# Kernel optimization log

Measured on AMD Instinct MI355X. Metric: run time of the kernel, lower is better.

## Reference

```python
import jax, jax.numpy as jnp
import numpy as np
from jax import lax

# pywt db4 filters. REC_LO is pywt's rec_lo; the others follow pywt's QMF relations:
# rec_hi[k] = (-1)**k * rec_lo[F-1-k]; dec_lo = rec_lo[::-1]; dec_hi = rec_hi[::-1].
REC_LO = np.array([0.23037781330885523, 0.7148465705525415, 0.6308807679295904,
                   -0.027983769416983849, -0.18703481171888114, 0.030841381835986965,
                   0.032883011666982945, -0.010597401784997278], dtype=np.float32)
F = 8
REC_HI = np.array([(-1.0) ** k * REC_LO[F - 1 - k] for k in range(F)], dtype=np.float32)
DEC_LO = REC_LO[::-1].copy()
DEC_HI = REC_HI[::-1].copy()
LEVELS = 3


def _conv(x, kern, stride=1, lhs_dilation=1, padding=((0, 0),)):
    # x: (N, 1, L) ; 1-D correlation (jax conv does NOT flip the kernel)
    k = jnp.asarray(kern, x.dtype).reshape(1, 1, -1)
    return lax.conv_general_dilated(x, k, window_strides=(stride,), padding=padding,
                                    lhs_dilation=(lhs_dilation,),
                                    dimension_numbers=('NCH', 'OIH', 'NCH'))


def dwt(x):
    # pywt single-level dwt, mode='symmetric': extend by F-1 each side, then
    # decimated convolution with dec filters. Equivalent to: drop first extended
    # sample and stride-2 correlate with reversed dec filter (= rec filter).
    xe = jnp.pad(x, ((0, 0), (0, 0), (F - 1, F - 1)), mode='symmetric')[..., 1:]
    cA = _conv(xe, REC_LO, stride=2)   # rev(DEC_LO) == REC_LO
    cD = _conv(xe, REC_HI, stride=2)   # rev(DEC_HI) == REC_HI
    return cA, cD


def idwt(a, d):
    # pywt idwt: upsample by 2 (zeros between samples, len 2L-1), full-convolve
    # with rec filters, trim F-2 from each side -> len 2L - F + 2.
    # Via dilated conv: lhs_dilation=2, pad 1 each side, correlate with rev(rec)=dec.
    ra = _conv(a, DEC_LO, lhs_dilation=2, padding=((1, 1),))
    rd = _conv(d, DEC_HI, lhs_dilation=2, padding=((1, 1),))
    return ra + rd


def waverec(coeffs):
    a = coeffs[0]
    for d in coeffs[1:]:
        if a.shape[-1] == d.shape[-1] + 1:
            a = a[..., :-1]
        a = idwt(a, d)
    return a


def setup_inputs() -> dict:
    key = jax.random.key(0)
    x = jax.random.normal(key, (32, 64, 8192), dtype=jnp.float32)
    return {"x": x}


def reference(x):
    B, C, n = x.shape
    a = x.reshape(B * C, 1, n)
    details = []
    for _ in range(LEVELS):
        a, d = dwt(a)
        details.append(d)
    coeffs = [a] + details[::-1]  # [cA_L, cD_L, ..., cD_1] as in pywt.wavedec
    bands = []
    for i in range(LEVELS + 1):
        kept = [c if j == i else jnp.zeros_like(c) for j, c in enumerate(coeffs)]
        rec = waverec(kept)[..., :n]
        bands.append(rec.reshape(B, C, n))
    return tuple(bands)
```

## Files before the change

### kernel.cpp

```cpp
#include <hip/hip_runtime.h>


#define T     256
#define N0    8192
#define L1    4099
#define L2    2053
#define L3    1030
#define NROWS 2048

#define RL0 0.23037781330885523f
#define RL1 0.7148465705525415f
#define RL2 0.6308807679295904f
#define RL3 (-0.02798376941698385f)
#define RL4 (-0.18703481171888114f)
#define RL5 0.030841381835986965f
#define RL6 0.032883011666982945f
#define RL7 (-0.010597401784997278f)

__device__ __forceinline__ void fwd_level(const float* __restrict__ src, int n, int Lout,
                                          float* __restrict__ dstA, float* __restrict__ dstD,
                                          int tid)
{
    const float lo[8] = {RL0, RL1, RL2, RL3, RL4, RL5, RL6, RL7};
    const float hi[8] = {RL7, -RL6, RL5, -RL4, RL3, -RL2, RL1, -RL0};
    for (int i = tid; i < Lout; i += T) {
        int j0 = 2 * i - 6;
        float sa = 0.f, sd = 0.f;
#pragma unroll
        for (int t = 0; t < 8; ++t) {
            int m = j0 + t;
            m = (m < 0) ? (-1 - m) : m;
            m = (m >= n) ? (2 * n - 1 - m) : m;
            float v = src[m];
            sa = fmaf(v, lo[t], sa);
            sd = fmaf(v, hi[t], sd);
        }
        dstA[i] = sa;
        dstD[i] = sd;
    }
}

__device__ __forceinline__ void upconv_mid(const float* __restrict__ s, float* __restrict__ dst,
                                           int L,
                                           float o0, float o1, float o2, float o3,
                                           float e0, float e1, float e2, float e3,
                                           int tid)
{
    for (int p = tid; p < L - 3; p += T) {
        float s0 = s[p], s1 = s[p + 1], s2 = s[p + 2], s3 = s[p + 3];
        float ev = s0 * e0 + s1 * e1 + s2 * e2 + s3 * e3;
        float od = s0 * o0 + s1 * o1 + s2 * o2 + s3 * o3;
        *(float2*)&dst[2 * p] = make_float2(ev, od);
    }
}

__device__ __forceinline__ void upconv_final(const float* __restrict__ s, float* __restrict__ gout,
                                             float o0, float o1, float o2, float o3,
                                             float e0, float e1, float e2, float e3,
                                             int tid)
{
    for (int q = tid; q < N0 / 4; q += T) {
        int p = 2 * q;
        float s0 = s[p], s1 = s[p + 1], s2 = s[p + 2], s3 = s[p + 3], s4 = s[p + 4];
        float4 o;
        o.x = s0 * e0 + s1 * e1 + s2 * e2 + s3 * e3;
        o.y = s0 * o0 + s1 * o1 + s2 * o2 + s3 * o3;
        o.z = s1 * e0 + s2 * e1 + s3 * e2 + s4 * e3;
        o.w = s1 * o0 + s2 * o1 + s3 * o2 + s4 * o3;
        ((float4*)gout)[q] = o;
    }
}

#define POOL_F 12312

__global__ __launch_bounds__(T) void wavelet_bands(const float* __restrict__ x,
                                                   float* __restrict__ out)
{
    __shared__ float buf[POOL_F];
    const int tid = threadIdx.x;
    const int row = blockIdx.x;

    float* a1 = buf;
    float* t2 = buf;
    float* d1 = buf + 4100;
    float* a2 = buf + 4100;
    float* t1 = buf + 4100;
    float* d2 = buf + 8199;
    float* a3 = buf + 10252;
    float* d3 = buf + 11282;

    const float* xr = x + (size_t)row * N0;
    const size_t band = (size_t)NROWS * N0;
    float* o0 = out + (size_t)row * N0;
    float* o1 = o0 + band;
    float* o2 = o0 + 2 * band;
    float* o3 = o0 + 3 * band;


    fwd_level(xr, N0, L1, a1, d1, tid);
    __syncthreads();

    upconv_final(d1, o3, -RL0, -RL2, -RL4, -RL6, RL1, RL3, RL5, RL7, tid);
    __syncthreads();

    fwd_level(a1, L1, L2, a2, d2, tid);
    __syncthreads();

    fwd_level(a2, L2, L3, a3, d3, tid);
    __syncthreads();

    upconv_mid(d2, t2, L2, -RL0, -RL2, -RL4, -RL6, RL1, RL3, RL5, RL7, tid);
    __syncthreads();
    upconv_final(t2, o2, RL7, RL5, RL3, RL1, RL6, RL4, RL2, RL0, tid);
    __syncthreads();

    upconv_mid(a3, t1, L3, RL7, RL5, RL3, RL1, RL6, RL4, RL2, RL0, tid);
    __syncthreads();
    upconv_mid(t1, t2, L2, RL7, RL5, RL3, RL1, RL6, RL4, RL2, RL0, tid);
    __syncthreads();
    upconv_final(t2, o0, RL7, RL5, RL3, RL1, RL6, RL4, RL2, RL0, tid);
    __syncthreads();

    upconv_mid(d3, t1, L3, -RL0, -RL2, -RL4, -RL6, RL1, RL3, RL5, RL7, tid);
    __syncthreads();
    upconv_mid(t1, t2, L2, RL7, RL5, RL3, RL1, RL6, RL4, RL2, RL0, tid);
    __syncthreads();
    upconv_final(t2, o1, RL7, RL5, RL3, RL1, RL6, RL4, RL2, RL0, tid);
}

extern "C" void kernel_launch(void* const* d_in, const int* in_sizes, int n_in,
                              void* d_out, int out_size, void* d_ws, size_t ws_size,
                              hipStream_t stream)
{
    const float* x = (const float*)d_in[0];
    float* out = (float*)d_out;
    wavelet_bands<<<NROWS, T, 0, stream>>>(x, out);
}
```

Baseline: 348.2 us.

## Quadruple block size, vectorize LDS access, split edges, merge independent stages between barriers

Raises threads per block from 256 to 1024. The forward DWT is split into a branch-free interior path, which computes two outputs per thread from float2 loads, and a separate symmetric-edge path. The upsampling convolutions now use float2 loads and float4 stores. The shared-memory layout is widened so that independent stages (forward level and upconv, final output and the next mid stage) can run between the same barriers, cutting the barrier count. More LDS per block and 1024-thread blocks may reduce blocks per CU, and the block-wide barriers get more costly.

```diff
diff --git a/kernel.cpp b/kernel.cpp
--- a/kernel.cpp
+++ b/kernel.cpp
@@ -1,7 +1,7 @@
 #include <hip/hip_runtime.h>
 
 
-#define T     256
+#define T     1024
 #define N0    8192
 #define L1    4099
 #define L2    2053
@@ -17,13 +17,40 @@
 #define RL6 0.032883011666982945f
 #define RL7 (-0.010597401784997278f)
 
-__device__ __forceinline__ void fwd_level(const float* __restrict__ src, int n, int Lout,
-                                          float* __restrict__ dstA, float* __restrict__ dstD,
-                                          int tid)
+__device__ __forceinline__ void fwd_interior(const float* __restrict__ s, int tHi,
+                                             float* __restrict__ dstA,
+                                             float* __restrict__ dstD, int tid)
 {
     const float lo[8] = {RL0, RL1, RL2, RL3, RL4, RL5, RL6, RL7};
     const float hi[8] = {RL7, -RL6, RL5, -RL4, RL3, -RL2, RL1, -RL0};
-    for (int i = tid; i < Lout; i += T) {
+    const float2* s2 = (const float2*)s;
+    for (int t = 2 + tid; t < tHi; t += T) {
+        float2 w0 = s2[2 * t - 3], w1 = s2[2 * t - 2], w2 = s2[2 * t - 1],
+               w3 = s2[2 * t],     w4 = s2[2 * t + 1];
+        float w[10] = {w0.x, w0.y, w1.x, w1.y, w2.x, w2.y, w3.x, w3.y, w4.x, w4.y};
+        float sa0 = 0.f, sd0 = 0.f, sa1 = 0.f, sd1 = 0.f;
+#pragma unroll
+        for (int k = 0; k < 8; ++k) {
+            sa0 = fmaf(w[k],     lo[k], sa0);
+            sd0 = fmaf(w[k],     hi[k], sd0);
+            sa1 = fmaf(w[k + 2], lo[k], sa1);
+            sd1 = fmaf(w[k + 2], hi[k], sd1);
+        }
+        ((float2*)dstA)[t] = make_float2(sa0, sa1);
+        ((float2*)dstD)[t] = make_float2(sd0, sd1);
+    }
+}
+
+__device__ __forceinline__ void fwd_edges(const float* __restrict__ s, int n, int Lout, int tHi,
+                                          float* __restrict__ dstA,
+                                          float* __restrict__ dstD, int tid)
+{
+    const float lo[8] = {RL0, RL1, RL2, RL3, RL4, RL5, RL6, RL7};
+    const float hi[8] = {RL7, -RL6, RL5, -RL4, RL3, -RL2, RL1, -RL0};
+    const int ub = 2 * tHi;
+    const int tot = 4 + (Lout - ub);
+    if (tid < tot) {
+        int i = (tid < 4) ? tid : ub + (tid - 4);
         int j0 = 2 * i - 6;
         float sa = 0.f, sd = 0.f;
 #pragma unroll
@@ -31,7 +58,7 @@
             int m = j0 + t;
             m = (m < 0) ? (-1 - m) : m;
             m = (m >= n) ? (2 * n - 1 - m) : m;
-            float v = src[m];
+            float v = s[m];
             sa = fmaf(v, lo[t], sa);
             sd = fmaf(v, hi[t], sd);
         }
@@ -43,35 +70,48 @@
 __device__ __forceinline__ void upconv_mid(const float* __restrict__ s, float* __restrict__ dst,
                                            int L,
                                            float o0, float o1, float o2, float o3,
-                                           float e0, float e1, float e2, float e3,
-                                           int tid)
+                                           float e0, float e1, float e2, float e3, int tid)
 {
-    for (int p = tid; p < L - 3; p += T) {
-        float s0 = s[p], s1 = s[p + 1], s2 = s[p + 2], s3 = s[p + 3];
-        float ev = s0 * e0 + s1 * e1 + s2 * e2 + s3 * e3;
-        float od = s0 * o0 + s1 * o1 + s2 * o2 + s3 * o3;
+    const float2* s2 = (const float2*)s;
+    const int cnt = L - 3, P2 = cnt >> 1;
+    for (int t = tid; t < P2; t += T) {
+        float2 u0 = s2[t], u1 = s2[t + 1];
+        float s4 = s[2 * t + 4];
+        float a0 = u0.x, a1 = u0.y, a2 = u1.x, a3 = u1.y;
+        float ev0 = a0 * e0 + a1 * e1 + a2 * e2 + a3 * e3;
+        float od0 = a0 * o0 + a1 * o1 + a2 * o2 + a3 * o3;
+        float ev1 = a1 * e0 + a2 * e1 + a3 * e2 + s4 * e3;
+        float od1 = a1 * o0 + a2 * o1 + a3 * o2 + s4 * o3;
+        ((float4*)dst)[t] = make_float4(ev0, od0, ev1, od1);
+    }
+    if ((cnt & 1) && tid == 0) {
+        int p = cnt - 1;
+        float s0 = s[p], s1 = s[p + 1], sc = s[p + 2], s3 = s[p + 3];
+        float ev = s0 * e0 + s1 * e1 + sc * e2 + s3 * e3;
+        float od = s0 * o0 + s1 * o1 + sc * o2 + s3 * o3;
         *(float2*)&dst[2 * p] = make_float2(ev, od);
     }
 }
 
-__device__ __forceinline__ void upconv_final(const float* __restrict__ s, float* __restrict__ gout,
+__device__ __forceinline__ void upconv_final(const float* __restrict__ s, float* __restrict__ g,
                                              float o0, float o1, float o2, float o3,
-                                             float e0, float e1, float e2, float e3,
-                                             int tid)
+                                             float e0, float e1, float e2, float e3, int tid)
 {
+    const float2* s2 = (const float2*)s;
     for (int q = tid; q < N0 / 4; q += T) {
-        int p = 2 * q;
-        float s0 = s[p], s1 = s[p + 1], s2 = s[p + 2], s3 = s[p + 3], s4 = s[p + 4];
+        float2 u0 = s2[q], u1 = s2[q + 1];
+        float s4 = s[2 * q + 4];
+        float a0 = u0.x, a1 = u0.y, a2 = u1.x, a3 = u1.y;
         float4 o;
-        o.x = s0 * e0 + s1 * e1 + s2 * e2 + s3 * e3;
-        o.y = s0 * o0 + s1 * o1 + s2 * o2 + s3 * o3;
-        o.z = s1 * e0 + s2 * e1 + s3 * e2 + s4 * e3;
-        o.w = s1 * o0 + s2 * o1 + s3 * o2 + s4 * o3;
-        ((float4*)gout)[q] = o;
+        o.x = a0 * e0 + a1 * e1 + a2 * e2 + a3 * e3;
+        o.y = a0 * o0 + a1 * o1 + a2 * o2 + a3 * o3;
+        o.z = a1 * e0 + a2 * e1 + a3 * e2 + s4 * e3;
+        o.w = a1 * o0 + a2 * o1 + a3 * o2 + s4 * o3;
+        ((float4*)g)[q] = o;
     }
 }
 
-#define POOL_F 12312
+#define POOL_F 14376
 
 __global__ __launch_bounds__(T) void wavelet_bands(const float* __restrict__ x,
                                                    float* __restrict__ out)
@@ -83,11 +123,11 @@
     float* a1 = buf;
     float* t2 = buf;
     float* d1 = buf + 4100;
-    float* a2 = buf + 4100;
-    float* t1 = buf + 4100;
-    float* d2 = buf + 8199;
-    float* a3 = buf + 10252;
-    float* d3 = buf + 11282;
+    float* a2 = buf + 8200;
+    float* t1 = buf + 8200;
+    float* d2 = buf + 10256;
+    float* a3 = buf + 12312;
+    float* d3 = buf + 13344;
 
     const float* xr = x + (size_t)row * N0;
     const size_t band = (size_t)NROWS * N0;
@@ -96,35 +136,38 @@
     float* o2 = o0 + 2 * band;
     float* o3 = o0 + 3 * band;
 
+    const int tHi1 = (N0 - 3) >> 2;
+    const int tHi2 = (L1 - 3) >> 2;
+    const int tHi3 = (L2 - 3) >> 2;
 
-    fwd_level(xr, N0, L1, a1, d1, tid);
+    fwd_interior(xr, tHi1, a1, d1, tid);
+    fwd_edges(xr, N0, L1, tHi1, a1, d1, tid);
     __syncthreads();
 
     upconv_final(d1, o3, -RL0, -RL2, -RL4, -RL6, RL1, RL3, RL5, RL7, tid);
+    fwd_interior(a1, tHi2, a2, d2, tid);
+    fwd_edges(a1, L1, L2, tHi2, a2, d2, tid);
     __syncthreads();
 
-    fwd_level(a1, L1, L2, a2, d2, tid);
+    fwd_interior(a2, tHi3, a3, d3, tid);
+    fwd_edges(a2, L2, L3, tHi3, a3, d3, tid);
+    upconv_mid(d2, t2, L2, -RL0, -RL2, -RL4, -RL6, RL1, RL3, RL5, RL7, tid);
     __syncthreads();
 
-    fwd_level(a2, L2, L3, a3, d3, tid);
+    upconv_final(t2, o2, RL7, RL5, RL3, RL1, RL6, RL4, RL2, RL0, tid);
+    upconv_mid(a3, t1, L3, RL7, RL5, RL3, RL1, RL6, RL4, RL2, RL0, tid);
     __syncthreads();
 
-    upconv_mid(d2, t2, L2, -RL0, -RL2, -RL4, -RL6, RL1, RL3, RL5, RL7, tid);
-    __syncthreads();
-    upconv_final(t2, o2, RL7, RL5, RL3, RL1, RL6, RL4, RL2, RL0, tid);
+    upconv_mid(t1, t2, L2, RL7, RL5, RL3, RL1, RL6, RL4, RL2, RL0, tid);
     __syncthreads();
 
-    upconv_mid(a3, t1, L3, RL7, RL5, RL3, RL1, RL6, RL4, RL2, RL0, tid);
+    upconv_final(t2, o0, RL7, RL5, RL3, RL1, RL6, RL4, RL2, RL0, tid);
+    upconv_mid(d3, t1, L3, -RL0, -RL2, -RL4, -RL6, RL1, RL3, RL5, RL7, tid);
     __syncthreads();
+
     upconv_mid(t1, t2, L2, RL7, RL5, RL3, RL1, RL6, RL4, RL2, RL0, tid);
     __syncthreads();
-    upconv_final(t2, o0, RL7, RL5, RL3, RL1, RL6, RL4, RL2, RL0, tid);
-    __syncthreads();
 
-    upconv_mid(d3, t1, L3, -RL0, -RL2, -RL4, -RL6, RL1, RL3, RL5, RL7, tid);
-    __syncthreads();
-    upconv_mid(t1, t2, L2, RL7, RL5, RL3, RL1, RL6, RL4, RL2, RL0, tid);
-    __syncthreads();
     upconv_final(t2, o1, RL7, RL5, RL3, RL1, RL6, RL4, RL2, RL0, tid);
 }
 
```

Result: faster. 317.5 us (-8.8%).
